# Kernel tuning notes

Hardware: AMD Instinct MI355X
Metric: run time of the kernel (lower is better)

## Reference

```python
import jax, jax.numpy as jnp
import numpy as np

DIM = 768
NUM_HEADS = 12
HEAD_DIM = DIM // NUM_HEADS
SCALE = HEAD_DIM ** -0.5


def setup_inputs() -> dict:
    key = jax.random.key(0)
    ks = jax.random.split(key, 7)
    B, N = 4, 2048
    s = DIM ** -0.5
    return {
        "x": jax.random.normal(ks[0], (B, N, DIM), dtype=jnp.float32),
        "attn_bias": jax.random.normal(ks[1], (1, NUM_HEADS, N, N), dtype=jnp.float32),
        "Wq": jax.random.normal(ks[2], (DIM, DIM), dtype=jnp.float32) * s,
        "Wk": jax.random.normal(ks[3], (DIM, DIM), dtype=jnp.float32) * s,
        "Wv": jax.random.normal(ks[4], (DIM, DIM), dtype=jnp.float32) * s,
        "Wp": jax.random.normal(ks[5], (DIM, DIM), dtype=jnp.float32) * s,
        "bp": jax.random.normal(ks[6], (DIM,), dtype=jnp.float32) * 0.02,
    }


def reference(x, attn_bias, Wq, Wk, Wv, Wp, bp):
    B, N, C = x.shape
    # Linear layers use y = x @ W.T (torch convention); split heads: [B,H,N,D]
    def heads(y):
        return y.reshape(B, N, NUM_HEADS, HEAD_DIM).transpose(0, 2, 1, 3)
    q = heads(x @ Wq.T)
    k = heads(x @ Wk.T)
    v = heads(x @ Wv.T)
    attn = jnp.einsum("bhnd,bhmd->bhnm", q, k) * SCALE + attn_bias
    attn = jax.nn.softmax(attn, axis=-1)
    out = jnp.einsum("bhnm,bhmd->bhnd", attn, v)
    out = out.transpose(0, 2, 1, 3).reshape(B, N, C)
    return out @ Wp.T + bp
```

## Files before the change

kernel.cpp:

```cpp
#include <hip/hip_runtime.h>
#include <hip/hip_bf16.h>

#define NTOK 2048
#define NHEADS 12
#define HDIM 64
#define DIM 768
#define BATCH 4
#define QBLK 64
#define SC2_    0.18033688011112042f
#define LOG2E_  1.4426950408889634f
#define SHIFT2_ 23.083120654223415f

typedef __attribute__((ext_vector_type(8))) short short8;
typedef __attribute__((ext_vector_type(4))) float f32x4;

__device__ __forceinline__ short f2bf(float f) {
  union { float f; unsigned u; } v; v.f = f;
  unsigned r = v.u + 0x7fffu + ((v.u >> 16) & 1u);
  return (short)(r >> 16);
}

__device__ __forceinline__ f32x4 mfma_bf16(short8 a, short8 b, f32x4 c) {
  return __builtin_amdgcn_mfma_f32_16x16x32_bf16(a, b, c, 0, 0, 0);
}

__device__ __forceinline__ void gload_lds16(const void* g, void* l) {
  __builtin_amdgcn_global_load_lds((const __attribute__((address_space(1))) void*)g,
                                   (__attribute__((address_space(3))) void*)l, 16, 0, 0);
}

__device__ __forceinline__ float exp2_hw(float x) {
  float r; asm("v_exp_f32 %0, %1" : "=v"(r) : "v"(x)); return r;
}

__device__ __forceinline__ unsigned cvt_pk_bf16(float lo, float hi) {
  unsigned r; asm("v_cvt_pk_bf16_f32 %0, %1, %2" : "=v"(r) : "v"(lo), "v"(hi)); return r;
}

__global__ void cvt_x(const float* __restrict__ src, short* __restrict__ dst) {
  int i = blockIdx.x * 256 + threadIdx.x;
  float4 v = ((const float4*)src)[i];
  short4 o; o.x = f2bf(v.x); o.y = f2bf(v.y); o.z = f2bf(v.z); o.w = f2bf(v.w);
  ((short4*)dst)[i] = o;
}

__global__ void cvt_w(const float* __restrict__ w0, const float* __restrict__ w1,
                      const float* __restrict__ w2, const float* __restrict__ w3,
                      short* __restrict__ d0, short* __restrict__ d1,
                      short* __restrict__ d2, short* __restrict__ d3) {
  int i = blockIdx.x * 256 + threadIdx.x;
  const float* s = blockIdx.y == 0 ? w0 : blockIdx.y == 1 ? w1 : blockIdx.y == 2 ? w2 : w3;
  short* d = blockIdx.y == 0 ? d0 : blockIdx.y == 1 ? d1 : blockIdx.y == 2 ? d2 : d3;
  float4 v = ((const float4*)s)[i];
  short4 o; o.x = f2bf(v.x); o.y = f2bf(v.y); o.z = f2bf(v.z); o.w = f2bf(v.w);
  ((short4*)d)[i] = o;
}

__device__ __forceinline__ void gemm_mainloop(const short* __restrict__ A,
                                              const short* __restrict__ B,
                                              int mbase, int nbase,
                                              short* As, short* Bs,
                                              f32x4 (&acc)[4][4], int lane, int w) {
  int lr = lane & 15, lg = lane >> 4;
  int wr = w >> 1, wc = w & 1;
  for (int kb = 0; kb < DIM; kb += 64) {
    if (kb) __syncthreads();
#pragma unroll
    for (int c = 0; c < 4; ++c) {
      int row = w * 32 + c * 8 + (lane >> 3);
      int sch = (lane & 7) ^ (row & 7);
      gload_lds16(A + (size_t)(mbase + row) * DIM + kb + sch * 8, (char*)As + w * 4096 + c * 1024);
      gload_lds16(B + (size_t)(nbase + row) * DIM + kb + sch * 8, (char*)Bs + w * 4096 + c * 1024);
    }
    __syncthreads();
#pragma unroll
    for (int ks = 0; ks < 2; ++ks) {
      short8 af[4], bf[4];
#pragma unroll
      for (int i = 0; i < 4; ++i) {
        int row = wr * 64 + i * 16 + lr;
        int ch = (ks * 4 + lg) ^ (row & 7);
        af[i] = *(const short8*)(As + row * 64 + ch * 8);
      }
#pragma unroll
      for (int j = 0; j < 4; ++j) {
        int row = wc * 64 + j * 16 + lr;
        int ch = (ks * 4 + lg) ^ (row & 7);
        bf[j] = *(const short8*)(Bs + row * 64 + ch * 8);
      }
#pragma unroll
      for (int i = 0; i < 4; ++i)
#pragma unroll
        for (int j = 0; j < 4; ++j)
          acc[i][j] = mfma_bf16(af[i], bf[j], acc[i][j]);
    }
  }
}

__global__ __launch_bounds__(256, 2) void gemm_qkv(const short* __restrict__ xb,
    const short* __restrict__ wq, const short* __restrict__ wk, const short* __restrict__ wv,
    short* __restrict__ Qh, short* __restrict__ Kh, short* __restrict__ Vt) {
  __shared__ __align__(16) short As[128 * 64];
  __shared__ __align__(16) short Bs[128 * 64];
  int nt = blockIdx.x, mt = blockIdx.y, z = blockIdx.z;
  const short* B = z == 0 ? wq : (z == 1 ? wk : wv);
  int tid = threadIdx.x, lane = tid & 63, w = tid >> 6;
  f32x4 acc[4][4] = {};
  gemm_mainloop(xb, B, mt * 128, nt * 128, As, Bs, acc, lane, w);
  int lr = lane & 15, lg = lane >> 4, wr = w >> 1, wc = w & 1;
  if (z < 2) {
    short* dst = z == 0 ? Qh : Kh;
#pragma unroll
    for (int i = 0; i < 4; ++i)
#pragma unroll
      for (int j = 0; j < 4; ++j) {
        int m = mt * 128 + wr * 64 + i * 16 + lg * 4;
        int n = nt * 128 + wc * 64 + j * 16 + lr;
        int bb = m >> 11, nn = m & 2047, hh = n >> 6, d = n & 63;
        size_t base = (((size_t)bb * NHEADS + hh) * NTOK + nn) * HDIM + d;
#pragma unroll
        for (int r = 0; r < 4; ++r)
          dst[base + (size_t)r * HDIM] = f2bf(acc[i][j][r]);
      }
  } else {
#pragma unroll
    for (int i = 0; i < 4; ++i)
#pragma unroll
      for (int j = 0; j < 4; ++j) {
        int m = mt * 128 + wr * 64 + i * 16 + lg * 4;
        int n = nt * 128 + wc * 64 + j * 16 + lr;
        int bb = m >> 11, nn = m & 2047, hh = n >> 6, d = n & 63;
        short4 pk;
        pk.x = f2bf(acc[i][j][0]); pk.y = f2bf(acc[i][j][1]);
        pk.z = f2bf(acc[i][j][2]); pk.w = f2bf(acc[i][j][3]);
        *(short4*)(Vt + (((size_t)bb * NHEADS + hh) * HDIM + d) * NTOK + nn) = pk;
      }
  }
}

__global__ __launch_bounds__(256, 4) void attn_fused(const short* __restrict__ Qh,
    const short* __restrict__ Kh, const short* __restrict__ Vt,
    const float* __restrict__ bias, short* __restrict__ Ob) {
  __shared__ __align__(16) short Ks[2][64 * 64];
  __shared__ __align__(16) short Vs[2][64 * 64];
  __shared__ __align__(16) short Ps[4][16 * 64];
  int d0 = blockIdx.x;
  int wg = (d0 & 7) * 192 + (d0 >> 3);
  int b = wg & 3, qb = (wg >> 2) & 31, h = wg >> 7;
  int tid = threadIdx.x, lane = tid & 63, w = tid >> 6;
  int lr = lane & 15, lg = lane >> 4;

  const short* Q = Qh + ((size_t)b * NHEADS + h) * NTOK * HDIM;
  const short* K = Kh + ((size_t)b * NHEADS + h) * NTOK * HDIM;
  const short* V = Vt + ((size_t)b * NHEADS + h) * HDIM * NTOK;
  const float* Bb = bias + ((size_t)h * NTOK + qb * QBLK + w * 16) * NTOK + (size_t)lr * NTOK;

  short8 qf[2];
  {
    const short* qp = Q + (size_t)(qb * QBLK + w * 16 + lr) * HDIM + lg * 8;
    qf[0] = *(const short8*)qp;
    qf[1] = *(const short8*)(qp + 32);
  }

  float psum = 0.f;
  f32x4 oacc[4] = {};
  short* myP = (short*)Ps[w];

  auto stage = [&](int buf, int kv) {
#pragma unroll
    for (int c = 0; c < 2; ++c) {
      int row = w * 16 + c * 8 + (lane >> 3);
      int sch = (lane & 7) ^ (row & 7);
      gload_lds16(K + (size_t)(kv + row) * HDIM + sch * 8, (char*)Ks[buf] + w * 2048 + c * 1024);
      gload_lds16(V + (size_t)row * NTOK + kv + sch * 8, (char*)Vs[buf] + w * 2048 + c * 1024);
    }
  };

  auto loadBias = [&](int kv, f32x4 (&bv)[4]) {
#pragma unroll
    for (int ni = 0; ni < 4; ++ni) {
      f32x4 v = *(const f32x4*)(Bb + kv + ni * 16 + lg * 4);
      bv[ni] = v * LOG2E_ - SHIFT2_;
    }
  };

  f32x4 bvA[4], bvB[4];
  loadBias(0, bvA);
  stage(0, 0);
  __syncthreads();

  auto body = [&](int t, int cur, f32x4 (&bvc)[4], f32x4 (&bvn)[4]) {
    int kv = t * 64;
    if (t < NTOK / 64 - 1) {
      stage(cur ^ 1, kv + 64);
      loadBias(kv + 64, bvn);
    }

    f32x4 sacc[4];
#pragma unroll
    for (int ni = 0; ni < 4; ++ni) sacc[ni] = (f32x4){0.f, 0.f, 0.f, 0.f};
    __builtin_amdgcn_s_setprio(1);
#pragma unroll
    for (int ni = 0; ni < 4; ++ni) {
      int row = ni * 16 + lr;
      short8 kf0 = *(const short8*)(Ks[cur] + row * 64 + ((lg ^ (row & 7)) * 8));
      short8 kf1 = *(const short8*)(Ks[cur] + row * 64 + (((4 + lg) ^ (row & 7)) * 8));
      sacc[ni] = mfma_bf16(kf0, qf[0], sacc[ni]);
      sacc[ni] = mfma_bf16(kf1, qf[1], sacc[ni]);
    }
    __builtin_amdgcn_s_setprio(0);

#pragma unroll
    for (int ni = 0; ni < 4; ++ni) {
      float p0 = exp2_hw(fmaf(sacc[ni][0], SC2_, bvc[ni][0]));
      float p1 = exp2_hw(fmaf(sacc[ni][1], SC2_, bvc[ni][1]));
      float p2 = exp2_hw(fmaf(sacc[ni][2], SC2_, bvc[ni][2]));
      float p3 = exp2_hw(fmaf(sacc[ni][3], SC2_, bvc[ni][3]));
      psum += (p0 + p1) + (p2 + p3);
      unsigned w0 = cvt_pk_bf16(p0, p1);
      unsigned w1 = cvt_pk_bf16(p2, p3);
      int colb = (ni * 16 + lg * 4) ^ ((lr & 7) << 3);
      *(unsigned*)(myP + lr * 64 + colb) = w0;
      *(unsigned*)(myP + lr * 64 + colb + 2) = w1;
    }

    short8 pf0 = *(const short8*)(myP + lr * 64 + ((lg ^ (lr & 7)) * 8));
    short8 pf1 = *(const short8*)(myP + lr * 64 + (((4 + lg) ^ (lr & 7)) * 8));
    __builtin_amdgcn_s_setprio(1);
#pragma unroll
    for (int ni = 0; ni < 4; ++ni) {
      int row = ni * 16 + lr;
      short8 vf0 = *(const short8*)(Vs[cur] + row * 64 + ((lg ^ (row & 7)) * 8));
      short8 vf1 = *(const short8*)(Vs[cur] + row * 64 + (((4 + lg) ^ (row & 7)) * 8));
      oacc[ni] = mfma_bf16(pf0, vf0, oacc[ni]);
      oacc[ni] = mfma_bf16(pf1, vf1, oacc[ni]);
    }
    __builtin_amdgcn_s_setprio(0);

    __syncthreads();
  };

  for (int t = 0; t < NTOK / 64; t += 2) {
    body(t, 0, bvA, bvB);
    body(t + 1, 1, bvB, bvA);
  }

  float ps = psum;
  ps += __shfl_xor(ps, 16);
  ps += __shfl_xor(ps, 32);
  float inv[4];
#pragma unroll
  for (int r = 0; r < 4; ++r)
    inv[r] = 1.f / __shfl(ps, lg * 4 + r);

#pragma unroll
  for (int r = 0; r < 4; ++r) {
    size_t orow = ((size_t)b * NTOK + qb * QBLK + w * 16 + lg * 4 + r) * DIM + h * HDIM;
#pragma unroll
    for (int ni = 0; ni < 4; ++ni)
      Ob[orow + ni * 16 + lr] = f2bf(oacc[ni][r] * inv[r]);
  }
}

__global__ __launch_bounds__(256, 2) void gemm_proj(const short* __restrict__ Ob,
    const short* __restrict__ wp, const float* __restrict__ bp, float* __restrict__ out) {
  __shared__ __align__(16) short As[128 * 64];
  __shared__ __align__(16) short Bs[128 * 64];
  int nt = blockIdx.x, mt = blockIdx.y;
  int tid = threadIdx.x, lane = tid & 63, w = tid >> 6;
  f32x4 acc[4][4] = {};
  gemm_mainloop(Ob, wp, mt * 128, nt * 128, As, Bs, acc, lane, w);
  int lr = lane & 15, lg = lane >> 4, wr = w >> 1, wc = w & 1;
#pragma unroll
  for (int j = 0; j < 4; ++j) {
    int n = nt * 128 + wc * 64 + j * 16 + lr;
    float bpv = bp[n];
#pragma unroll
    for (int i = 0; i < 4; ++i) {
      int m = mt * 128 + wr * 64 + i * 16 + lg * 4;
#pragma unroll
      for (int r = 0; r < 4; ++r)
        out[(size_t)(m + r) * DIM + n] = acc[i][j][r] + bpv;
    }
  }
}

extern "C" void kernel_launch(void* const* d_in, const int* in_sizes, int n_in,
                              void* d_out, int out_size, void* d_ws, size_t ws_size,
                              hipStream_t stream) {
  const float* x    = (const float*)d_in[0];
  const float* bias = (const float*)d_in[1];
  const float* Wq   = (const float*)d_in[2];
  const float* Wk   = (const float*)d_in[3];
  const float* Wv   = (const float*)d_in[4];
  const float* Wp   = (const float*)d_in[5];
  const float* bp   = (const float*)d_in[6];
  float* out = (float*)d_out;

  char* ws = (char*)d_ws;
  short* xb  = (short*)(ws);
  short* wqb = (short*)(ws + 12582912);
  short* wkb = (short*)(ws + 13762560);
  short* wvb = (short*)(ws + 14942208);
  short* wpb = (short*)(ws + 16121856);
  short* Qh  = (short*)(ws + 17301504);
  short* Kh  = (short*)(ws + 29884416);
  short* Vt  = (short*)(ws + 42467328);
  short* Ob  = (short*)(ws + 55050240);

  cvt_x<<<6144, 256, 0, stream>>>(x, xb);
  cvt_w<<<dim3(576, 4), 256, 0, stream>>>(Wq, Wk, Wv, Wp, wqb, wkb, wvb, wpb);
  gemm_qkv<<<dim3(6, 64, 3), 256, 0, stream>>>(xb, wqb, wkb, wvb, Qh, Kh, Vt);
  attn_fused<<<1536, 256, 0, stream>>>(Qh, Kh, Vt, bias, Ob);
  gemm_proj<<<dim3(6, 64), 256, 0, stream>>>(Ob, wpb, bp, out);
}
```

Baseline: 220.4 us.

## Switch attention to 32x32 MFMA with register-resident P and bias-initialized scores

The attention kernel now uses 32x32x16 bf16 MFMA and gives each wave 32 query rows, so a block covers 128 queries and the grid drops from 1536 to 768 blocks. The P tile no longer goes through shared memory: it is rearranged across lanes with permlane32_swap to form the second MFMA operand directly. The bias is loaded into the score accumulator before the QK MFMA, pre-scaled so that one multiply before exp2 yields the same fixed-shift exponent as before. The aim is to reuse each staged K/V tile across more queries and to remove the LDS write and read of P. The cost is more registers per thread, with launch bounds lowered to 3 blocks per CU, and less overlap, because the bias loads are no longer prefetched one iteration ahead.

```diff
diff --git a/kernel.cpp b/kernel.cpp
--- a/kernel.cpp
+++ b/kernel.cpp
@@ -6,13 +6,11 @@
 #define HDIM 64
 #define DIM 768
 #define BATCH 4
-#define QBLK 64
-#define SC2_    0.18033688011112042f
-#define LOG2E_  1.4426950408889634f
-#define SHIFT2_ 23.083120654223415f
+#define SC2_ 0.18033688011112042f
 
 typedef __attribute__((ext_vector_type(8))) short short8;
 typedef __attribute__((ext_vector_type(4))) float f32x4;
+typedef __attribute__((ext_vector_type(16))) float f32x16;
 
 __device__ __forceinline__ short f2bf(float f) {
   union { float f; unsigned u; } v; v.f = f;
@@ -22,6 +20,10 @@
 
 __device__ __forceinline__ f32x4 mfma_bf16(short8 a, short8 b, f32x4 c) {
   return __builtin_amdgcn_mfma_f32_16x16x32_bf16(a, b, c, 0, 0, 0);
+}
+
+__device__ __forceinline__ f32x16 mfma32(short8 a, short8 b, f32x16 c) {
+  return __builtin_amdgcn_mfma_f32_32x32x16_bf16(a, b, c, 0, 0, 0);
 }
 
 __device__ __forceinline__ void gload_lds16(const void* g, void* l) {
@@ -138,128 +140,123 @@
   }
 }
 
-__global__ __launch_bounds__(256, 4) void attn_fused(const short* __restrict__ Qh,
+__global__ __launch_bounds__(256, 3) void attn_fused(const short* __restrict__ Qh,
     const short* __restrict__ Kh, const short* __restrict__ Vt,
     const float* __restrict__ bias, short* __restrict__ Ob) {
   __shared__ __align__(16) short Ks[2][64 * 64];
   __shared__ __align__(16) short Vs[2][64 * 64];
-  __shared__ __align__(16) short Ps[4][16 * 64];
   int d0 = blockIdx.x;
-  int wg = (d0 & 7) * 192 + (d0 >> 3);
-  int b = wg & 3, qb = (wg >> 2) & 31, h = wg >> 7;
+  int wg = (d0 & 7) * 96 + (d0 >> 3);
+  int b = wg & 3, qb = (wg >> 2) & 15, h = wg >> 6;
   int tid = threadIdx.x, lane = tid & 63, w = tid >> 6;
-  int lr = lane & 15, lg = lane >> 4;
+  int ql = lane & 31, hi = lane >> 5, sx = ql & 7;
 
   const short* Q = Qh + ((size_t)b * NHEADS + h) * NTOK * HDIM;
   const short* K = Kh + ((size_t)b * NHEADS + h) * NTOK * HDIM;
   const short* V = Vt + ((size_t)b * NHEADS + h) * HDIM * NTOK;
-  const float* Bb = bias + ((size_t)h * NTOK + qb * QBLK + w * 16) * NTOK + (size_t)lr * NTOK;
-
-  short8 qf[2];
-  {
-    const short* qp = Q + (size_t)(qb * QBLK + w * 16 + lr) * HDIM + lg * 8;
-    qf[0] = *(const short8*)qp;
-    qf[1] = *(const short8*)(qp + 32);
-  }
+  int qrow = qb * 128 + w * 32 + ql;
+  const float* Bb = bias + ((size_t)h * NTOK + qrow) * NTOK;
+
+  short8 qf[4];
+#pragma unroll
+  for (int i = 0; i < 4; ++i)
+    qf[i] = *(const short8*)(Q + (size_t)qrow * HDIM + i * 16 + hi * 8);
 
   float psum = 0.f;
-  f32x4 oacc[4] = {};
-  short* myP = (short*)Ps[w];
+  f32x16 oacc[2] = {};
 
   auto stage = [&](int buf, int kv) {
 #pragma unroll
     for (int c = 0; c < 2; ++c) {
       int row = w * 16 + c * 8 + (lane >> 3);
-      int sch = (lane & 7) ^ (row & 7);
+      int sch = (lane & 7) ^ (lane >> 3);
       gload_lds16(K + (size_t)(kv + row) * HDIM + sch * 8, (char*)Ks[buf] + w * 2048 + c * 1024);
       gload_lds16(V + (size_t)row * NTOK + kv + sch * 8, (char*)Vs[buf] + w * 2048 + c * 1024);
     }
   };
 
-  auto loadBias = [&](int kv, f32x4 (&bv)[4]) {
-#pragma unroll
-    for (int ni = 0; ni < 4; ++ni) {
-      f32x4 v = *(const f32x4*)(Bb + kv + ni * 16 + lg * 4);
-      bv[ni] = v * LOG2E_ - SHIFT2_;
-    }
-  };
-
-  f32x4 bvA[4], bvB[4];
-  loadBias(0, bvA);
   stage(0, 0);
   __syncthreads();
 
-  auto body = [&](int t, int cur, f32x4 (&bvc)[4], f32x4 (&bvn)[4]) {
+  auto body = [&](int t, int cur) {
     int kv = t * 64;
-    if (t < NTOK / 64 - 1) {
-      stage(cur ^ 1, kv + 64);
-      loadBias(kv + 64, bvn);
-    }
-
-    f32x4 sacc[4];
-#pragma unroll
-    for (int ni = 0; ni < 4; ++ni) sacc[ni] = (f32x4){0.f, 0.f, 0.f, 0.f};
+
+    f32x16 sacc[2];
+#pragma unroll
+    for (int kb = 0; kb < 2; ++kb)
+#pragma unroll
+      for (int g = 0; g < 4; ++g) {
+        f32x4 bb = *(const f32x4*)(Bb + kv + kb * 32 + g * 8 + hi * 4);
+#pragma unroll
+        for (int r = 0; r < 4; ++r)
+          sacc[kb][g * 4 + r] = fmaf(bb[r], 8.f, -128.f);
+      }
+
+    if (t < NTOK / 64 - 1) stage(cur ^ 1, kv + 64);
+
     __builtin_amdgcn_s_setprio(1);
 #pragma unroll
-    for (int ni = 0; ni < 4; ++ni) {
-      int row = ni * 16 + lr;
-      short8 kf0 = *(const short8*)(Ks[cur] + row * 64 + ((lg ^ (row & 7)) * 8));
-      short8 kf1 = *(const short8*)(Ks[cur] + row * 64 + (((4 + lg) ^ (row & 7)) * 8));
-      sacc[ni] = mfma_bf16(kf0, qf[0], sacc[ni]);
-      sacc[ni] = mfma_bf16(kf1, qf[1], sacc[ni]);
-    }
+    for (int kb = 0; kb < 2; ++kb)
+#pragma unroll
+      for (int i = 0; i < 4; ++i) {
+        short8 kf = *(const short8*)(Ks[cur] + (kb * 32 + ql) * 64 + (((i * 2 + hi) ^ sx) * 8));
+        sacc[kb] = mfma32(kf, qf[i], sacc[kb]);
+      }
     __builtin_amdgcn_s_setprio(0);
 
 #pragma unroll
-    for (int ni = 0; ni < 4; ++ni) {
-      float p0 = exp2_hw(fmaf(sacc[ni][0], SC2_, bvc[ni][0]));
-      float p1 = exp2_hw(fmaf(sacc[ni][1], SC2_, bvc[ni][1]));
-      float p2 = exp2_hw(fmaf(sacc[ni][2], SC2_, bvc[ni][2]));
-      float p3 = exp2_hw(fmaf(sacc[ni][3], SC2_, bvc[ni][3]));
-      psum += (p0 + p1) + (p2 + p3);
-      unsigned w0 = cvt_pk_bf16(p0, p1);
-      unsigned w1 = cvt_pk_bf16(p2, p3);
-      int colb = (ni * 16 + lg * 4) ^ ((lr & 7) << 3);
-      *(unsigned*)(myP + lr * 64 + colb) = w0;
-      *(unsigned*)(myP + lr * 64 + colb + 2) = w1;
-    }
-
-    short8 pf0 = *(const short8*)(myP + lr * 64 + ((lg ^ (lr & 7)) * 8));
-    short8 pf1 = *(const short8*)(myP + lr * 64 + (((4 + lg) ^ (lr & 7)) * 8));
-    __builtin_amdgcn_s_setprio(1);
-#pragma unroll
-    for (int ni = 0; ni < 4; ++ni) {
-      int row = ni * 16 + lr;
-      short8 vf0 = *(const short8*)(Vs[cur] + row * 64 + ((lg ^ (row & 7)) * 8));
-      short8 vf1 = *(const short8*)(Vs[cur] + row * 64 + (((4 + lg) ^ (row & 7)) * 8));
-      oacc[ni] = mfma_bf16(pf0, vf0, oacc[ni]);
-      oacc[ni] = mfma_bf16(pf1, vf1, oacc[ni]);
-    }
-    __builtin_amdgcn_s_setprio(0);
+    for (int kb = 0; kb < 2; ++kb) {
+      float p[16];
+#pragma unroll
+      for (int rg = 0; rg < 16; ++rg) p[rg] = exp2_hw(sacc[kb][rg] * SC2_);
+      float ts = 0.f;
+#pragma unroll
+      for (int g = 0; g < 4; ++g)
+        ts += (p[g * 4] + p[g * 4 + 1]) + (p[g * 4 + 2] + p[g * 4 + 3]);
+      psum += ts;
+      unsigned Wd[4][2];
+#pragma unroll
+      for (int g = 0; g < 4; ++g)
+#pragma unroll
+        for (int tt = 0; tt < 2; ++tt)
+          Wd[g][tt] = cvt_pk_bf16(p[g * 4 + tt * 2], p[g * 4 + tt * 2 + 1]);
+
+#pragma unroll
+      for (int cc = 0; cc < 2; ++cc) {
+        auto r0 = __builtin_amdgcn_permlane32_swap(Wd[cc * 2][0], Wd[cc * 2 + 1][0], false, false);
+        auto r1 = __builtin_amdgcn_permlane32_swap(Wd[cc * 2][1], Wd[cc * 2 + 1][1], false, false);
+        union { unsigned u[4]; short8 s; } pb;
+        pb.u[0] = r0[0]; pb.u[1] = r1[0]; pb.u[2] = r0[1]; pb.u[3] = r1[1];
+        __builtin_amdgcn_s_setprio(1);
+#pragma unroll
+        for (int db = 0; db < 2; ++db) {
+          short8 vf = *(const short8*)(Vs[cur] + (db * 32 + ql) * 64 + (((kb * 4 + cc * 2 + hi) ^ sx) * 8));
+          oacc[db] = mfma32(vf, pb.s, oacc[db]);
+        }
+        __builtin_amdgcn_s_setprio(0);
+      }
+    }
 
     __syncthreads();
   };
 
   for (int t = 0; t < NTOK / 64; t += 2) {
-    body(t, 0, bvA, bvB);
-    body(t + 1, 1, bvB, bvA);
+    body(t, 0);
+    body(t + 1, 1);
   }
 
-  float ps = psum;
-  ps += __shfl_xor(ps, 16);
-  ps += __shfl_xor(ps, 32);
-  float inv[4];
-#pragma unroll
-  for (int r = 0; r < 4; ++r)
-    inv[r] = 1.f / __shfl(ps, lg * 4 + r);
-
-#pragma unroll
-  for (int r = 0; r < 4; ++r) {
-    size_t orow = ((size_t)b * NTOK + qb * QBLK + w * 16 + lg * 4 + r) * DIM + h * HDIM;
-#pragma unroll
-    for (int ni = 0; ni < 4; ++ni)
-      Ob[orow + ni * 16 + lr] = f2bf(oacc[ni][r] * inv[r]);
-  }
+  float fs = psum + __shfl_xor(psum, 32);
+  float inv = 1.f / fs;
+  size_t obase = ((size_t)b * NTOK + qrow) * DIM + h * HDIM;
+#pragma unroll
+  for (int db = 0; db < 2; ++db)
+#pragma unroll
+    for (int g = 0; g < 4; ++g) {
+      unsigned u0 = cvt_pk_bf16(oacc[db][g * 4] * inv, oacc[db][g * 4 + 1] * inv);
+      unsigned u1 = cvt_pk_bf16(oacc[db][g * 4 + 2] * inv, oacc[db][g * 4 + 3] * inv);
+      uint2 pk; pk.x = u0; pk.y = u1;
+      *(uint2*)(Ob + obase + db * 32 + g * 8 + hi * 4) = pk;
+    }
 }
 
 __global__ __launch_bounds__(256, 2) void gemm_proj(const short* __restrict__ Ob,
@@ -311,6 +308,6 @@
   cvt_x<<<6144, 256, 0, stream>>>(x, xb);
   cvt_w<<<dim3(576, 4), 256, 0, stream>>>(Wq, Wk, Wv, Wp, wqb, wkb, wvb, wpb);
   gemm_qkv<<<dim3(6, 64, 3), 256, 0, stream>>>(xb, wqb, wkb, wvb, Qh, Kh, Vt);
-  attn_fused<<<1536, 256, 0, stream>>>(Qh, Kh, Vt, bias, Ob);
+  attn_fused<<<768, 256, 0, stream>>>(Qh, Kh, Vt, bias, Ob);
   gemm_proj<<<dim3(6, 64), 256, 0, stream>>>(Ob, wpb, bp, out);
 }
```

Result: faster. 214.7 us (-2.6%).
